# Kernel optimization log

Measured on AMD Instinct MI355X. Metric: run time of the kernel, lower is better.

## Reference

```python
import jax, jax.numpy as jnp
import numpy as np

B, N, D, H = 2, 256, 512, 8
DK = D // H


def _lin(x, w, b):
    # torch nn.Linear: y = x @ W.T + b, W is [out, in]
    return jnp.matmul(x, w.T) + b


def setup_inputs() -> dict:
    key = jax.random.key(0)
    ks = jax.random.split(key, 12)
    std = 0.02
    inp = {
        "x": jax.random.normal(ks[0], (B, N, D), jnp.float32),
        "batched_graphs": jax.random.normal(ks[1], (B, N, N, D), jnp.float32) * std,
        "mask": jnp.zeros((B, N, N), dtype=bool),
    }
    names = ["wq", "wk", "wv", "wo", "wl", "wr", "wrk", "wrv"]
    for i, n in enumerate(names):
        inp[n] = jax.random.normal(ks[2 + i], (D, D), jnp.float32) * std
        inp["b" + n[1:]] = jnp.zeros((D,), jnp.float32)
    return inp


def reference(x, batched_graphs, mask,
              wq, bq, wk, bk, wv, bv, wo, bo,
              wl, bl, wr, br, wrk, brk, wrv, brv):
    # update_relations: per-edge key/value maps
    graphs_k = _lin(batched_graphs, wrk, brk).reshape(B, N, N, H, DK)
    graphs_v = _lin(batched_graphs, wrv, brv).reshape(B, N, N, H, DK)

    query = _lin(x, wq, bq).reshape(B, N, H, DK)
    key_ = _lin(x, wk, bk).reshape(B, N, H, DK)
    value = _lin(x, wv, bv).reshape(B, N, H, DK)

    scores_k = jnp.einsum("bxhd,byhd->bxyh", query, key_)
    scores_g = jnp.einsum("bxhd,bxyhd->bxyh", query, graphs_k)
    scores = (scores_k + scores_g) / np.sqrt(DK).astype(np.float32)
    scores = jnp.where(mask[..., None], jnp.float32(-1e9), scores)
    p_attn = jax.nn.softmax(scores, axis=2)  # over key nodes y

    x_v = jnp.einsum("bxyh,byhd->bxhd", p_attn, value)
    x_g = jnp.einsum("bxyh,bxyhd->bxhd", p_attn, graphs_v)
    out = (x_v + x_g).reshape(B, N, D)

    # relation update: outer sum of left/right projections
    x_left = _lin(out, wl, bl)[:, :, None, :]   # [B,N,1,D]
    x_right = _lin(out, wr, br)[:, None, :, :]  # [B,1,N,D]
    new_graphs = x_left + x_right               # [B,N,N,D]

    return _lin(out, wo, bo), new_graphs
```

## Files before the change

### kernel.cpp

```cpp
#include <hip/hip_runtime.h>

#define BB 2
#define NN 256
#define DD 512
#define HH 8

typedef float f4raw __attribute__((ext_vector_type(4)));

__device__ __forceinline__ float dot4(float4 a, float4 b) {
    return a.x*b.x + a.y*b.y + a.z*b.z + a.w*b.w;
}

__device__ __forceinline__ float4 f4fma(float s, float4 a, float4 acc) {
    acc.x += s * a.x; acc.y += s * a.y; acc.z += s * a.z; acc.w += s * a.w;
    return acc;
}

__device__ __forceinline__ float4 f4mul(float s, float4 a) {
    a.x *= s; a.y *= s; a.z *= s; a.w *= s; return a;
}

__device__ __forceinline__ void gload_lds16(const void* g, void* l) {
    __builtin_amdgcn_global_load_lds(
        (const __attribute__((address_space(1))) unsigned int*)g,
        (__attribute__((address_space(3))) unsigned int*)l, 16, 0, 0);
}

__device__ __forceinline__ void stage_swz(const char* rowbase, float4* dst, int w, int lane) {
    #pragma unroll
    for (int j = 0; j < 4; ++j) {
        const int f0 = w * 256 + j * 64;
        const int y = f0 >> 7;
        const int c = (f0 & 127) + lane;
        gload_lds16(rowbase + (size_t)y * 2048 + ((size_t)(c ^ y) << 4), &dst[f0]);
    }
}

__device__ __forceinline__ void stageG(const char* Grow, int tt, int w, int lane, float4* dst) {
    #pragma unroll
    for (int r = 0; r < 2; ++r) {
        const int yr = 2 * w + r;
        const char* src = Grow + (size_t)(tt * 8 + yr) * 2048;
        #pragma unroll
        for (int j = 0; j < 2; ++j) {
            const int c = j * 64 + lane;
            gload_lds16(src + ((size_t)(c ^ yr) << 4), &dst[r * 128 + j * 64]);
        }
    }
}

__global__ __launch_bounds__(64) void kProj(
    const float* __restrict__ in_,
    const float* __restrict__ w0, const float* __restrict__ b0,
    const float* __restrict__ w1, const float* __restrict__ b1,
    const float* __restrict__ w2, const float* __restrict__ b2,
    float* __restrict__ o0, float* __restrict__ o1, float* __restrict__ o2)
{
    __shared__ float4 xs[2][32 * 5];
    __shared__ float4 ws[2][32 * 5];

    const int t = threadIdx.x;
    const int blk = blockIdx.x;
    const int proj = blk >> 8;
    const int rem = blk & 255;
    const int row0 = (rem >> 4) * 32;
    const int col0 = (rem & 15) * 32;

    const float* W; const float* Bp; float* O;
    if (proj == 0)      { W = w0; Bp = b0; O = o0; }
    else if (proj == 1) { W = w1; Bp = b1; O = o1; }
    else                { W = w2; Bp = b2; O = o2; }

    const float4* X4 = (const float4*)in_ + (size_t)row0 * 128;
    const float4* W4 = (const float4*)W  + (size_t)col0 * 128;

    const int sr = t >> 2, se = t & 3;
    const int ty = t >> 3, tx = t & 7;

    float4 rx0 = X4[(size_t)sr * 128 + se];
    float4 rx1 = X4[(size_t)(sr + 16) * 128 + se];
    float4 rw0 = W4[(size_t)sr * 128 + se];
    float4 rw1 = W4[(size_t)(sr + 16) * 128 + se];
    xs[0][sr * 5 + se] = rx0;  xs[0][(sr + 16) * 5 + se] = rx1;
    ws[0][sr * 5 + se] = rw0;  ws[0][(sr + 16) * 5 + se] = rw1;

    float acc[4][4] = {};

    for (int q = 0; q < 32; ++q) {
        __syncthreads();
        const int cur = q & 1;
        if (q < 31) {
            const int ko = (q + 1) * 4;
            rx0 = X4[(size_t)sr * 128 + ko + se];
            rx1 = X4[(size_t)(sr + 16) * 128 + ko + se];
            rw0 = W4[(size_t)sr * 128 + ko + se];
            rw1 = W4[(size_t)(sr + 16) * 128 + ko + se];
        }
        const float4* xb = xs[cur];
        const float4* wb = ws[cur];
        #pragma unroll
        for (int e4 = 0; e4 < 4; ++e4) {
            float4 xr[4], wc[4];
            #pragma unroll
            for (int i = 0; i < 4; ++i) xr[i] = xb[(ty + 8 * i) * 5 + e4];
            #pragma unroll
            for (int j = 0; j < 4; ++j) wc[j] = wb[(tx + 8 * j) * 5 + e4];
            #pragma unroll
            for (int i = 0; i < 4; ++i)
                #pragma unroll
                for (int j = 0; j < 4; ++j)
                    acc[i][j] += dot4(xr[i], wc[j]);
        }
        if (q < 31) {
            const int nxt = cur ^ 1;
            xs[nxt][sr * 5 + se] = rx0;  xs[nxt][(sr + 16) * 5 + se] = rx1;
            ws[nxt][sr * 5 + se] = rw0;  ws[nxt][(sr + 16) * 5 + se] = rw1;
        }
    }

    float bb[4];
    #pragma unroll
    for (int j = 0; j < 4; ++j) bb[j] = Bp[col0 + tx + 8 * j];
    #pragma unroll
    for (int i = 0; i < 4; ++i) {
        const int orow = row0 + ty + 8 * i;
        #pragma unroll
        for (int j = 0; j < 4; ++j)
            O[(size_t)orow * DD + col0 + tx + 8 * j] = acc[i][j] + bb[j];
    }
}

__global__ __launch_bounds__(256) void kQkp(
    const float* __restrict__ q, const float* __restrict__ wrk,
    float* __restrict__ qkp)
{
    __shared__ float qs[8 * 64];
    const int t = threadIdx.x;
    const int blk = blockIdx.x;
    const int rowg = blk >> 5;
    const int h = (blk >> 2) & 7;
    const int eq = blk & 3;
    const int row0 = rowg * 8;
    {
        const int r = t >> 5, d2 = (t & 31) * 2;
        const float2 tmp = *(const float2*)(q + (size_t)(row0 + r) * DD + h * 64 + d2);
        qs[r * 64 + d2] = tmp.x; qs[r * 64 + d2 + 1] = tmp.y;
    }
    __syncthreads();
    const int e = eq * 128 + (t & 127);
    const int rp = (t >> 7) * 4;
    const float* wcol = wrk + (size_t)(h * 64) * DD + e;
    float a0 = 0, a1 = 0, a2 = 0, a3 = 0;
    #pragma unroll 8
    for (int d = 0; d < 64; ++d) {
        const float wv = wcol[(size_t)d * DD];
        a0 += qs[(rp + 0) * 64 + d] * wv;
        a1 += qs[(rp + 1) * 64 + d] * wv;
        a2 += qs[(rp + 2) * 64 + d] * wv;
        a3 += qs[(rp + 3) * 64 + d] * wv;
    }
    qkp[((size_t)(row0 + rp + 0) * HH + h) * DD + e] = a0;
    qkp[((size_t)(row0 + rp + 1) * HH + h) * DD + e] = a1;
    qkp[((size_t)(row0 + rp + 2) * HH + h) * DD + e] = a2;
    qkp[((size_t)(row0 + rp + 3) * HH + h) * DD + e] = a3;
}

__global__ __launch_bounds__(256) void kSk(
    const float* __restrict__ q, const float* __restrict__ k,
    const unsigned char* __restrict__ mask, float* __restrict__ sk)
{
    __shared__ float qs[8 * 65];
    __shared__ float ks[64 * 65];
    const int t = threadIdx.x;
    const int blk = blockIdx.x;
    const int b  = blk >> 10;
    const int h  = (blk >> 7) & 7;
    const int xt = (blk >> 2) & 31;
    const int yt = blk & 3;
    const int x0 = xt * 8, y0 = yt * 64;
    {
        const int r = t >> 5, d2 = (t & 31) * 2;
        const float2 tmp = *(const float2*)(q + (size_t)(b * NN + x0 + r) * DD + h * 64 + d2);
        qs[r * 65 + d2] = tmp.x; qs[r * 65 + d2 + 1] = tmp.y;
    }
    #pragma unroll
    for (int j = 0; j < 8; ++j) {
        const int f = t + 256 * j;
        const int r = f >> 5, d2 = (f & 31) * 2;
        const float2 tmp = *(const float2*)(k + (size_t)(b * NN + y0 + r) * DD + h * 64 + d2);
        ks[r * 65 + d2] = tmp.x; ks[r * 65 + d2 + 1] = tmp.y;
    }
    __syncthreads();
    const int xi = t >> 5, yg = t & 31;
    float a0 = 0, a1 = 0;
    #pragma unroll 8
    for (int d = 0; d < 64; ++d) {
        const float qv = qs[xi * 65 + d];
        a0 += qv * ks[(yg * 2 + 0) * 65 + d];
        a1 += qv * ks[(yg * 2 + 1) * 65 + d];
    }
    a0 *= 0.125f; a1 *= 0.125f;
    const unsigned char* mrow = mask + (size_t)(b * NN + x0 + xi) * NN;
    const int gy = y0 + yg * 2;
    if (mrow[gy + 0]) a0 = -1e9f;
    if (mrow[gy + 1]) a1 = -1e9f;
    float2 st; st.x = a0; st.y = a1;
    *(float2*)(sk + ((size_t)(b * NN + x0 + xi) * HH + h) * NN + gy) = st;
}

__global__ __launch_bounds__(256, 2) void kC(
    const float* __restrict__ G, const float* __restrict__ sk,
    const float* __restrict__ qkp, const float* __restrict__ v,
    const float* __restrict__ wrv, const float* __restrict__ brv,
    float* __restrict__ om)
{
    __shared__ float4 Gdb[2][4][256];
    __shared__ float4 qk4[1024];
    __shared__ float  sk_l[2048];
    __shared__ float  s_st[2048];
    __shared__ float  ml[64];

    const int t = threadIdx.x;
    const int lane = t & 63;
    const int w = t >> 6;
    const int bid = blockIdx.x;
    const int b = bid >> 8;

    const char* Grow = (const char*)(G + (size_t)bid * NN * DD);

    stage_swz((const char*)(qkp + (size_t)bid * HH * DD), qk4, w, lane);
    {
        const char* skb = (const char*)(sk + (size_t)bid * HH * NN);
        gload_lds16(skb + (size_t)(w * 128 + lane) * 16,      (float4*)sk_l + w * 128);
        gload_lds16(skb + (size_t)(w * 128 + 64 + lane) * 16, (float4*)sk_l + w * 128 + 64);
    }
    stageG(Grow, 0, w, lane, &Gdb[0][w][0]);
    asm volatile("s_waitcnt vmcnt(4)" ::: "memory");
    __builtin_amdgcn_sched_barrier(0);
    __builtin_amdgcn_s_barrier();

    const int s_ = lane & 15;
    const int g  = lane >> 4;
    const int h0 = 2 * g;
    const int yr0 = 2 * w, yr1 = 2 * w + 1;

    float4 gA[8], gB[8];
    float m[8], l[8];
    #pragma unroll
    for (int h = 0; h < 8; ++h) {
        gA[h] = make_float4(0, 0, 0, 0); gB[h] = make_float4(0, 0, 0, 0);
        m[h] = -3e38f; l[h] = 0.f;
    }

    int cb = 0;
    #pragma unroll 1
    for (int tt = 0; tt < 32; ++tt) {
        __builtin_amdgcn_sched_barrier(0);
        if (tt < 31) {
            stageG(Grow, tt + 1, w, lane, &Gdb[cb ^ 1][w][0]);
            asm volatile("s_waitcnt vmcnt(4)" ::: "memory");
        } else {
            asm volatile("s_waitcnt vmcnt(0)" ::: "memory");
        }
        __builtin_amdgcn_sched_barrier(0);

        const float4* gb = &Gdb[cb][w][0];
        const int gy0 = tt * 8 + yr0, gy1 = tt * 8 + yr1;

        {
            float a00 = 0, a01 = 0, a10 = 0, a11 = 0;
            #pragma unroll
            for (int i = 0; i < 8; ++i) {
                const int e4 = i * 16 + s_;
                const float4 g0 = gb[(e4 ^ yr0)];
                const float4 g1 = gb[128 + (e4 ^ yr1)];
                const float4 p0 = qk4[h0 * 128 + (e4 ^ h0)];
                const float4 p1 = qk4[(h0 + 1) * 128 + (e4 ^ (h0 + 1))];
                a00 += dot4(g0, p0); a01 += dot4(g0, p1);
                a10 += dot4(g1, p0); a11 += dot4(g1, p1);
            }
            #pragma unroll
            for (int mm = 1; mm < 16; mm <<= 1) {
                a00 += __shfl_xor(a00, mm); a01 += __shfl_xor(a01, mm);
                a10 += __shfl_xor(a10, mm); a11 += __shfl_xor(a11, mm);
            }
            if (s_ < 4) {
                const int yy = s_ & 1, hh = s_ >> 1;
                const float val = yy ? (hh ? a11 : a10) : (hh ? a01 : a00);
                const int h = h0 + hh;
                const int gy = yy ? gy1 : gy0;
                s_st[gy * 8 + h] = val * 0.125f + sk_l[h * 256 + gy];
            }
        }

        const float4 sva = *(const float4*)&s_st[gy0 * 8];
        const float4 svb = *(const float4*)&s_st[gy0 * 8 + 4];
        const float4 svc = *(const float4*)&s_st[gy1 * 8];
        const float4 svd = *(const float4*)&s_st[gy1 * 8 + 4];
        const float s0[8] = {sva.x, sva.y, sva.z, sva.w, svb.x, svb.y, svb.z, svb.w};
        const float s1[8] = {svc.x, svc.y, svc.z, svc.w, svd.x, svd.y, svd.z, svd.w};

        const float4 gr0a = gb[(lane ^ yr0)];
        const float4 gr0b = gb[((lane + 64) ^ yr0)];
        const float4 gr1a = gb[128 + (lane ^ yr1)];
        const float4 gr1b = gb[128 + ((lane + 64) ^ yr1)];

        #pragma unroll
        for (int h = 0; h < 8; ++h) {
            const float mn = fmaxf(m[h], fmaxf(s0[h], s1[h]));
            const float rs = __expf(m[h] - mn);
            const float p0 = __expf(s0[h] - mn);
            const float p1 = __expf(s1[h] - mn);
            m[h] = mn;
            l[h] = l[h] * rs + p0 + p1;
            gA[h] = f4fma(p1, gr1a, f4fma(p0, gr0a, f4mul(rs, gA[h])));
            gB[h] = f4fma(p1, gr1b, f4fma(p0, gr0b, f4mul(rs, gB[h])));
        }
        cb ^= 1;
    }

    asm volatile("s_waitcnt vmcnt(0)" ::: "memory");
    __syncthreads();
    if (lane == 0) {
        #pragma unroll
        for (int h = 0; h < 8; ++h) { ml[w * 16 + h] = m[h]; ml[w * 16 + 8 + h] = l[h]; }
    }
    __syncthreads();

    float M[8], Lf[8];
    #pragma unroll
    for (int h = 0; h < 8; ++h) {
        const float m0 = ml[h], m1 = ml[16 + h], m2 = ml[32 + h], m3 = ml[48 + h];
        const float mm = fmaxf(fmaxf(m0, m1), fmaxf(m2, m3));
        M[h] = mm;
        Lf[h] = __expf(m0 - mm) * ml[8 + h]  + __expf(m1 - mm) * ml[24 + h]
              + __expf(m2 - mm) * ml[40 + h] + __expf(m3 - mm) * ml[56 + h];
    }
    #pragma unroll
    for (int h = 0; h < 8; ++h) {
        const float ws = __expf(m[h] - M[h]);
        gA[h] = f4mul(ws, gA[h]); gB[h] = f4mul(ws, gB[h]);
    }
    float4* rA = &Gdb[0][0][0];
    float4* rB = &Gdb[1][0][0];
    if (w == 2) {
        #pragma unroll
        for (int h = 0; h < 8; ++h) { rA[h * 128 + lane] = gA[h]; rA[h * 128 + 64 + lane] = gB[h]; }
    }
    if (w == 3) {
        #pragma unroll
        for (int h = 0; h < 8; ++h) { rB[h * 128 + lane] = gA[h]; rB[h * 128 + 64 + lane] = gB[h]; }
    }
    __syncthreads();
    if (w == 0) {
        #pragma unroll
        for (int h = 0; h < 8; ++h) {
            gA[h].x += rA[h*128+lane].x; gA[h].y += rA[h*128+lane].y; gA[h].z += rA[h*128+lane].z; gA[h].w += rA[h*128+lane].w;
            gB[h].x += rA[h*128+64+lane].x; gB[h].y += rA[h*128+64+lane].y; gB[h].z += rA[h*128+64+lane].z; gB[h].w += rA[h*128+64+lane].w;
        }
    }
    if (w == 1) {
        #pragma unroll
        for (int h = 0; h < 8; ++h) {
            gA[h].x += rB[h*128+lane].x; gA[h].y += rB[h*128+lane].y; gA[h].z += rB[h*128+lane].z; gA[h].w += rB[h*128+lane].w;
            gB[h].x += rB[h*128+64+lane].x; gB[h].y += rB[h*128+64+lane].y; gB[h].z += rB[h*128+64+lane].z; gB[h].w += rB[h*128+64+lane].w;
        }
    }
    __syncthreads();
    if (w == 1) {
        #pragma unroll
        for (int h = 0; h < 8; ++h) { rA[h * 128 + lane] = gA[h]; rA[h * 128 + 64 + lane] = gB[h]; }
    }
    __syncthreads();
    if (w == 0) {
        #pragma unroll
        for (int h = 0; h < 8; ++h) {
            gA[h].x += rA[h*128+lane].x; gA[h].y += rA[h*128+lane].y; gA[h].z += rA[h*128+lane].z; gA[h].w += rA[h*128+lane].w;
            gB[h].x += rA[h*128+64+lane].x; gB[h].y += rA[h*128+64+lane].y; gB[h].z += rA[h*128+64+lane].z; gB[h].w += rA[h*128+64+lane].w;
            qk4[h * 128 + lane] = gA[h];
            qk4[h * 128 + 64 + lane] = gB[h];
        }
    }
    if (t == 0) {
        #pragma unroll
        for (int h = 0; h < 8; ++h) ml[h] = Lf[h];
    }
    {
        #pragma unroll
        for (int h = 0; h < 8; ++h) sk_l[t * 8 + h] = __expf(s_st[t * 8 + h] - M[h]);
    }
    __syncthreads();

    const float* vb = v + (size_t)(b * NN) * DD;
    #pragma unroll
    for (int jj = 0; jj < 2; ++jj) {
        const int o = jj * 256 + t;
        const int h = o >> 6, d = o & 63;
        const float4* wr4 = (const float4*)(wrv + (size_t)o * DD);
        const float4* gf = (const float4*)qk4 + h * 128;
        float acc = 0;
        #pragma unroll 4
        for (int e4 = 0; e4 < 128; ++e4) acc += dot4(wr4[e4], gf[e4]);
        float xv = 0;
        const float* vc = vb + h * 64 + d;
        #pragma unroll 4
        for (int y = 0; y < 256; ++y) xv += sk_l[y * 8 + h] * vc[(size_t)y * DD];
        om[(size_t)bid * DD + o] = (xv + acc) / ml[h] + brv[o];
    }
}

__global__ __launch_bounds__(256) void kE(
    const float* __restrict__ xl, const float* __restrict__ xr,
    float* __restrict__ ng)
{
    const int t = threadIdx.x;
    const int blk = blockIdx.x;
    const int bid = blk >> 2;
    const int yc = blk & 3;
    const int b = bid >> 8;
    const int o4 = t & 127;
    const int yh = t >> 7;
    const float4 left = ((const float4*)xl)[(size_t)bid * 128 + o4];
    const float4* xr4 = (const float4*)xr + (size_t)b * NN * 128;
    f4raw* out4 = (f4raw*)ng + (size_t)bid * NN * 128;
    for (int y = yc * 64 + yh; y < yc * 64 + 64; y += 2) {
        const float4 rr = xr4[y * 128 + o4];
        f4raw s;
        s.x = left.x + rr.x; s.y = left.y + rr.y;
        s.z = left.z + rr.z; s.w = left.w + rr.w;
        __builtin_nontemporal_store(s, &out4[y * 128 + o4]);
    }
}

extern "C" void kernel_launch(void* const* d_in, const int* in_sizes, int n_in,
                              void* d_out, int out_size, void* d_ws, size_t ws_size,
                              hipStream_t stream)
{
    (void)in_sizes; (void)n_in; (void)out_size; (void)ws_size;
    const float* x    = (const float*)d_in[0];
    const float* G    = (const float*)d_in[1];
    const unsigned char* mask = (const unsigned char*)d_in[2];
    const float* wq  = (const float*)d_in[3];  const float* bq  = (const float*)d_in[4];
    const float* wk  = (const float*)d_in[5];  const float* bk  = (const float*)d_in[6];
    const float* wv  = (const float*)d_in[7];  const float* bv  = (const float*)d_in[8];
    const float* wo  = (const float*)d_in[9];  const float* bo  = (const float*)d_in[10];
    const float* wl  = (const float*)d_in[11]; const float* bl  = (const float*)d_in[12];
    const float* wr  = (const float*)d_in[13]; const float* br  = (const float*)d_in[14];
    const float* wrk = (const float*)d_in[15];
    const float* wrv = (const float*)d_in[17]; const float* brv = (const float*)d_in[18];

    float* out  = (float*)d_out;
    float* fout = out;
    float* ng   = out + (size_t)BB * NN * DD;

    const size_t ng_f  = (size_t)BB * NN * NN * DD;
    const size_t row_f = (size_t)BB * NN * DD;
    const size_t total = row_f * 16;
    float* base = ng + ng_f - total;
    float* q    = base;
    float* k    = q   + row_f;
    float* vv_  = k   + row_f;
    float* qkp  = vv_ + row_f;
    float* skp  = qkp + row_f * 8;
    float* om   = skp + row_f * 4;
    float* xl = (float*)d_ws;
    float* xr = xl + row_f;

    kProj<<<768, 64, 0, stream>>>(x, wq, bq, wk, bk, wv, bv, q, k, vv_);
    kQkp <<<2048, 256, 0, stream>>>(q, wrk, qkp);
    kSk  <<<2048, 256, 0, stream>>>(q, k, mask, skp);
    kC   <<<512, 256, 0, stream>>>(G, skp, qkp, vv_, wrv, brv, om);
    kProj<<<768, 64, 0, stream>>>(om, wo, bo, wl, bl, wr, br, fout, xl, xr);
    kE   <<<2048, 256, 0, stream>>>(xl, xr, ng);
}
```

Before: 291.4 us.

## Split attention over key chunks with flash-decoding style merge kernel

The main attention kernel kC now splits each query row's 256 keys into four 64-key partitions, launching 2048 blocks instead of 512. Each block writes partial graph-weighted sums, value sums, running max and denominators. A new kernel kM merges the four partials with rescaled exponentials and applies the wrv projection and bias. The value accumulation also moves into the streaming loop, replacing the separate post-loop pass over v. This raises parallelism on the bandwidth-bound G stream, at the cost of an extra launch and about 32 row-sized partial buffers written to and read from global scratch.

```diff
diff --git a/kernel.cpp b/kernel.cpp
--- a/kernel.cpp
+++ b/kernel.cpp
@@ -18,6 +18,10 @@
 
 __device__ __forceinline__ float4 f4mul(float s, float4 a) {
     a.x *= s; a.y *= s; a.z *= s; a.w *= s; return a;
+}
+
+__device__ __forceinline__ float4 f4add(float4 a, float4 b) {
+    a.x += b.x; a.y += b.y; a.z += b.z; a.w += b.w; return a;
 }
 
 __device__ __forceinline__ void gload_lds16(const void* g, void* l) {
@@ -211,61 +215,71 @@
 __global__ __launch_bounds__(256, 2) void kC(
     const float* __restrict__ G, const float* __restrict__ sk,
     const float* __restrict__ qkp, const float* __restrict__ v,
-    const float* __restrict__ wrv, const float* __restrict__ brv,
-    float* __restrict__ om)
+    float* __restrict__ pg, float* __restrict__ pxv,
+    float* __restrict__ pm, float* __restrict__ pl)
 {
     __shared__ float4 Gdb[2][4][256];
     __shared__ float4 qk4[1024];
-    __shared__ float  sk_l[2048];
-    __shared__ float  s_st[2048];
-    __shared__ float  ml[64];
+    __shared__ float  sk_lds[512];
+    __shared__ float  s_st[512];
 
     const int t = threadIdx.x;
     const int lane = t & 63;
     const int w = t >> 6;
-    const int bid = blockIdx.x;
+    const int blk = blockIdx.x;
+    const int part = blk & 3;
+    const int bid = blk >> 2;
     const int b = bid >> 8;
-
-    const char* Grow = (const char*)(G + (size_t)bid * NN * DD);
-
+    const int ybase = part * 64;
+
+    const int s_ = lane & 15;
+    const int g  = lane >> 4;
+    const int h0_ = 2 * g, h1_ = h0_ + 1;
+    const int yr0 = 2 * w, yr1 = yr0 + 1;
+
+    const char* Grow = (const char*)(G + (size_t)bid * NN * DD) + (size_t)ybase * 2048;
+    const float* skb = sk + (size_t)bid * HH * NN;
+    const float4* vb4 = (const float4*)(v + (size_t)(b * NN) * DD);
+
+    const int f0p = 2 * t, f1p = 2 * t + 1;
+    const float skv0 = skb[(f0p & 7) * NN + ybase + (f0p >> 3)];
+    const float skv1 = skb[(f1p & 7) * NN + ybase + (f1p >> 3)];
     stage_swz((const char*)(qkp + (size_t)bid * HH * DD), qk4, w, lane);
-    {
-        const char* skb = (const char*)(sk + (size_t)bid * HH * NN);
-        gload_lds16(skb + (size_t)(w * 128 + lane) * 16,      (float4*)sk_l + w * 128);
-        gload_lds16(skb + (size_t)(w * 128 + 64 + lane) * 16, (float4*)sk_l + w * 128 + 64);
-    }
     stageG(Grow, 0, w, lane, &Gdb[0][w][0]);
     asm volatile("s_waitcnt vmcnt(4)" ::: "memory");
     __builtin_amdgcn_sched_barrier(0);
-    __builtin_amdgcn_s_barrier();
-
-    const int s_ = lane & 15;
-    const int g  = lane >> 4;
-    const int h0 = 2 * g;
-    const int yr0 = 2 * w, yr1 = 2 * w + 1;
+    sk_lds[f0p] = skv0;
+    sk_lds[f1p] = skv1;
+    __syncthreads();
 
     float4 gA[8], gB[8];
     float m[8], l[8];
     #pragma unroll
     for (int h = 0; h < 8; ++h) {
-        gA[h] = make_float4(0, 0, 0, 0); gB[h] = make_float4(0, 0, 0, 0);
+        gA[h] = make_float4(0, 0, 0, 0);
+        gB[h] = make_float4(0, 0, 0, 0);
         m[h] = -3e38f; l[h] = 0.f;
     }
+    float4 xva = {0, 0, 0, 0}, xvb = {0, 0, 0, 0};
 
     int cb = 0;
     #pragma unroll 1
-    for (int tt = 0; tt < 32; ++tt) {
+    for (int tt = 0; tt < 8; ++tt) {
+        const int gy0 = ybase + tt * 8 + yr0;
+        const int gy1 = gy0 + 1;
+        const int ry0 = tt * 8 + yr0, ry1 = ry0 + 1;
+
+        const float4 va0 = vb4[(size_t)gy0 * 128 + 32 * g + s_];
+        const float4 vb0 = vb4[(size_t)gy0 * 128 + 32 * g + 16 + s_];
+        const float4 va1 = vb4[(size_t)gy1 * 128 + 32 * g + s_];
+        const float4 vb1 = vb4[(size_t)gy1 * 128 + 32 * g + 16 + s_];
         __builtin_amdgcn_sched_barrier(0);
-        if (tt < 31) {
+        if (tt < 7)
             stageG(Grow, tt + 1, w, lane, &Gdb[cb ^ 1][w][0]);
-            asm volatile("s_waitcnt vmcnt(4)" ::: "memory");
-        } else {
-            asm volatile("s_waitcnt vmcnt(0)" ::: "memory");
-        }
+        asm volatile("s_waitcnt vmcnt(4)" ::: "memory");
         __builtin_amdgcn_sched_barrier(0);
 
         const float4* gb = &Gdb[cb][w][0];
-        const int gy0 = tt * 8 + yr0, gy1 = tt * 8 + yr1;
 
         {
             float a00 = 0, a01 = 0, a10 = 0, a11 = 0;
@@ -274,8 +288,8 @@
                 const int e4 = i * 16 + s_;
                 const float4 g0 = gb[(e4 ^ yr0)];
                 const float4 g1 = gb[128 + (e4 ^ yr1)];
-                const float4 p0 = qk4[h0 * 128 + (e4 ^ h0)];
-                const float4 p1 = qk4[(h0 + 1) * 128 + (e4 ^ (h0 + 1))];
+                const float4 p0 = qk4[h0_ * 128 + (e4 ^ h0_)];
+                const float4 p1 = qk4[h1_ * 128 + (e4 ^ h1_)];
                 a00 += dot4(g0, p0); a01 += dot4(g0, p1);
                 a10 += dot4(g1, p0); a11 += dot4(g1, p1);
             }
@@ -287,16 +301,16 @@
             if (s_ < 4) {
                 const int yy = s_ & 1, hh = s_ >> 1;
                 const float val = yy ? (hh ? a11 : a10) : (hh ? a01 : a00);
-                const int h = h0 + hh;
-                const int gy = yy ? gy1 : gy0;
-                s_st[gy * 8 + h] = val * 0.125f + sk_l[h * 256 + gy];
+                const int h = h0_ + hh;
+                const int ry = yy ? ry1 : ry0;
+                s_st[ry * 8 + h] = val * 0.125f + sk_lds[ry * 8 + h];
             }
         }
 
-        const float4 sva = *(const float4*)&s_st[gy0 * 8];
-        const float4 svb = *(const float4*)&s_st[gy0 * 8 + 4];
-        const float4 svc = *(const float4*)&s_st[gy1 * 8];
-        const float4 svd = *(const float4*)&s_st[gy1 * 8 + 4];
+        const float4 sva = *(const float4*)&s_st[ry0 * 8];
+        const float4 svb = *(const float4*)&s_st[ry0 * 8 + 4];
+        const float4 svc = *(const float4*)&s_st[ry1 * 8];
+        const float4 svd = *(const float4*)&s_st[ry1 * 8 + 4];
         const float s0[8] = {sva.x, sva.y, sva.z, sva.w, svb.x, svb.y, svb.z, svb.w};
         const float s1[8] = {svc.x, svc.y, svc.z, svc.w, svd.x, svd.y, svd.z, svd.w};
 
@@ -305,6 +319,7 @@
         const float4 gr1a = gb[128 + (lane ^ yr1)];
         const float4 gr1b = gb[128 + ((lane + 64) ^ yr1)];
 
+        float p0a = 0, p1a = 0, rsa = 1, p0b = 0, p1b = 0, rsb = 1;
         #pragma unroll
         for (int h = 0; h < 8; ++h) {
             const float mn = fmaxf(m[h], fmaxf(s0[h], s1[h]));
@@ -315,34 +330,46 @@
             l[h] = l[h] * rs + p0 + p1;
             gA[h] = f4fma(p1, gr1a, f4fma(p0, gr0a, f4mul(rs, gA[h])));
             gB[h] = f4fma(p1, gr1b, f4fma(p0, gr0b, f4mul(rs, gB[h])));
-        }
+            if (h == h0_) { p0a = p0; p1a = p1; rsa = rs; }
+            if (h == h1_) { p0b = p0; p1b = p1; rsb = rs; }
+        }
+        xva = f4fma(p1a, va1, f4fma(p0a, va0, f4mul(rsa, xva)));
+        xvb = f4fma(p1b, vb1, f4fma(p0b, vb0, f4mul(rsb, xvb)));
         cb ^= 1;
     }
 
     asm volatile("s_waitcnt vmcnt(0)" ::: "memory");
     __syncthreads();
+    float* ml = sk_lds;
     if (lane == 0) {
         #pragma unroll
         for (int h = 0; h < 8; ++h) { ml[w * 16 + h] = m[h]; ml[w * 16 + 8 + h] = l[h]; }
     }
     __syncthreads();
 
-    float M[8], Lf[8];
+    float ea = 1.f, eb = 1.f;
+    float Mv[8], Lv[8];
     #pragma unroll
     for (int h = 0; h < 8; ++h) {
-        const float m0 = ml[h], m1 = ml[16 + h], m2 = ml[32 + h], m3 = ml[48 + h];
-        const float mm = fmaxf(fmaxf(m0, m1), fmaxf(m2, m3));
-        M[h] = mm;
-        Lf[h] = __expf(m0 - mm) * ml[8 + h]  + __expf(m1 - mm) * ml[24 + h]
-              + __expf(m2 - mm) * ml[40 + h] + __expf(m3 - mm) * ml[56 + h];
-    }
-    #pragma unroll
-    for (int h = 0; h < 8; ++h) {
-        const float ws = __expf(m[h] - M[h]);
-        gA[h] = f4mul(ws, gA[h]); gB[h] = f4mul(ws, gB[h]);
-    }
+        const float q0 = ml[h], q1 = ml[16 + h], q2 = ml[32 + h], q3 = ml[48 + h];
+        const float Mh = fmaxf(fmaxf(q0, q1), fmaxf(q2, q3));
+        const float Lh = __expf(q0 - Mh) * ml[8 + h]  + __expf(q1 - Mh) * ml[24 + h]
+                       + __expf(q2 - Mh) * ml[40 + h] + __expf(q3 - Mh) * ml[56 + h];
+        Mv[h] = Mh; Lv[h] = Lh;
+        const float e = __expf(m[h] - Mh);
+        gA[h] = f4mul(e, gA[h]);
+        gB[h] = f4mul(e, gB[h]);
+        if (h == h0_) ea = e;
+        if (h == h1_) eb = e;
+    }
+    xva = f4mul(ea, xva);
+    xvb = f4mul(eb, xvb);
+
     float4* rA = &Gdb[0][0][0];
     float4* rB = &Gdb[1][0][0];
+    float4* xs_ = qk4;
+    xs_[w * 128 + 32 * g + s_] = xva;
+    xs_[w * 128 + 32 * g + 16 + s_] = xvb;
     if (w == 2) {
         #pragma unroll
         for (int h = 0; h < 8; ++h) { rA[h * 128 + lane] = gA[h]; rA[h * 128 + 64 + lane] = gB[h]; }
@@ -355,15 +382,15 @@
     if (w == 0) {
         #pragma unroll
         for (int h = 0; h < 8; ++h) {
-            gA[h].x += rA[h*128+lane].x; gA[h].y += rA[h*128+lane].y; gA[h].z += rA[h*128+lane].z; gA[h].w += rA[h*128+lane].w;
-            gB[h].x += rA[h*128+64+lane].x; gB[h].y += rA[h*128+64+lane].y; gB[h].z += rA[h*128+64+lane].z; gB[h].w += rA[h*128+64+lane].w;
+            gA[h] = f4add(gA[h], rA[h * 128 + lane]);
+            gB[h] = f4add(gB[h], rA[h * 128 + 64 + lane]);
         }
     }
     if (w == 1) {
         #pragma unroll
         for (int h = 0; h < 8; ++h) {
-            gA[h].x += rB[h*128+lane].x; gA[h].y += rB[h*128+lane].y; gA[h].z += rB[h*128+lane].z; gA[h].w += rB[h*128+lane].w;
-            gB[h].x += rB[h*128+64+lane].x; gB[h].y += rB[h*128+64+lane].y; gB[h].z += rB[h*128+64+lane].z; gB[h].w += rB[h*128+64+lane].w;
+            gA[h] = f4add(gA[h], rB[h * 128 + lane]);
+            gB[h] = f4add(gB[h], rB[h * 128 + 64 + lane]);
         }
     }
     __syncthreads();
@@ -373,40 +400,92 @@
     }
     __syncthreads();
     if (w == 0) {
+        float4* pgb = (float4*)pg + (size_t)blk * 1024;
         #pragma unroll
         for (int h = 0; h < 8; ++h) {
-            gA[h].x += rA[h*128+lane].x; gA[h].y += rA[h*128+lane].y; gA[h].z += rA[h*128+lane].z; gA[h].w += rA[h*128+lane].w;
-            gB[h].x += rA[h*128+64+lane].x; gB[h].y += rA[h*128+64+lane].y; gB[h].z += rA[h*128+64+lane].z; gB[h].w += rA[h*128+64+lane].w;
-            qk4[h * 128 + lane] = gA[h];
-            qk4[h * 128 + 64 + lane] = gB[h];
-        }
-    }
-    if (t == 0) {
-        #pragma unroll
-        for (int h = 0; h < 8; ++h) ml[h] = Lf[h];
+            gA[h] = f4add(gA[h], rA[h * 128 + lane]);
+            gB[h] = f4add(gB[h], rA[h * 128 + 64 + lane]);
+            pgb[h * 128 + lane] = gA[h];
+            pgb[h * 128 + 64 + lane] = gB[h];
+        }
+        float4 xa = f4add(f4add(xs_[32 * g + s_],            xs_[128 + 32 * g + s_]),
+                          f4add(xs_[256 + 32 * g + s_],      xs_[384 + 32 * g + s_]));
+        float4 xb = f4add(f4add(xs_[32 * g + 16 + s_],       xs_[128 + 32 * g + 16 + s_]),
+                          f4add(xs_[256 + 32 * g + 16 + s_], xs_[384 + 32 * g + 16 + s_]));
+        float4* pxb = (float4*)pxv + (size_t)blk * 128;
+        pxb[32 * g + s_] = xa;
+        pxb[32 * g + 16 + s_] = xb;
+        if (lane == 0) {
+            #pragma unroll
+            for (int h = 0; h < 8; ++h) { pm[blk * 8 + h] = Mv[h]; pl[blk * 8 + h] = Lv[h]; }
+        }
+    }
+}
+
+__global__ __launch_bounds__(256) void kM(
+    const float* __restrict__ pg, const float* __restrict__ pxv,
+    const float* __restrict__ pm, const float* __restrict__ pl,
+    const float* __restrict__ wrv, const float* __restrict__ brv,
+    float* __restrict__ om)
+{
+    __shared__ float4 gc[512];
+    __shared__ float xvs[256];
+    __shared__ float wexp[16], Ls[4];
+    const int t = threadIdx.x;
+    const int blk = blockIdx.x;
+    const int bid = blk >> 1;
+    const int half = blk & 1;
+    const int h0 = half * 4;
+    __shared__ float mlds[16], llds[16];
+    if (t < 16) {
+        const int i = t >> 2, hh = t & 3;
+        mlds[t] = pm[bid * 32 + i * 8 + h0 + hh];
+        llds[t] = pl[bid * 32 + i * 8 + h0 + hh];
+    }
+    __syncthreads();
+    if (t < 4) {
+        float M = mlds[t];
+        #pragma unroll
+        for (int i = 1; i < 4; ++i) M = fmaxf(M, mlds[i * 4 + t]);
+        float L = 0;
+        #pragma unroll
+        for (int i = 0; i < 4; ++i) {
+            const float wv = __expf(mlds[i * 4 + t] - M);
+            wexp[i * 4 + t] = wv;
+            L += wv * llds[i * 4 + t];
+        }
+        Ls[t] = L;
+    }
+    __syncthreads();
+    const int c4 = t & 127;
+    #pragma unroll
+    for (int r = 0; r < 2; ++r) {
+        const int hh = (t >> 7) * 2 + r;
+        float4 acc = {0, 0, 0, 0};
+        #pragma unroll
+        for (int i = 0; i < 4; ++i) {
+            const float wv = wexp[i * 4 + hh];
+            const float4 g = ((const float4*)pg)[((size_t)bid * 4 + i) * 1024 + (size_t)(h0 + hh) * 128 + c4];
+            acc.x += wv * g.x; acc.y += wv * g.y; acc.z += wv * g.z; acc.w += wv * g.w;
+        }
+        gc[hh * 128 + c4] = acc;
     }
     {
-        #pragma unroll
-        for (int h = 0; h < 8; ++h) sk_l[t * 8 + h] = __expf(s_st[t * 8 + h] - M[h]);
-    }
-    __syncthreads();
-
-    const float* vb = v + (size_t)(b * NN) * DD;
-    #pragma unroll
-    for (int jj = 0; jj < 2; ++jj) {
-        const int o = jj * 256 + t;
-        const int h = o >> 6, d = o & 63;
-        const float4* wr4 = (const float4*)(wrv + (size_t)o * DD);
-        const float4* gf = (const float4*)qk4 + h * 128;
-        float acc = 0;
-        #pragma unroll 4
-        for (int e4 = 0; e4 < 128; ++e4) acc += dot4(wr4[e4], gf[e4]);
-        float xv = 0;
-        const float* vc = vb + h * 64 + d;
-        #pragma unroll 4
-        for (int y = 0; y < 256; ++y) xv += sk_l[y * 8 + h] * vc[(size_t)y * DD];
-        om[(size_t)bid * DD + o] = (xv + acc) / ml[h] + brv[o];
-    }
+        const int hh = t >> 6;
+        float s = 0;
+        #pragma unroll
+        for (int i = 0; i < 4; ++i)
+            s += wexp[i * 4 + hh] * pxv[((size_t)bid * 4 + i) * DD + half * 256 + t];
+        xvs[t] = s;
+    }
+    __syncthreads();
+    const int o = half * 256 + t;
+    const int hl = t >> 6;
+    const float4* wr4 = (const float4*)(wrv + (size_t)o * DD);
+    float acc = 0;
+    #pragma unroll 4
+    for (int e4 = 0; e4 < 128; ++e4) acc += dot4(wr4[e4], gc[hl * 128 + e4]);
+    om[(size_t)bid * DD + o] = (xvs[t] + acc) / Ls[hl] + brv[o];
 }
 
 __global__ __launch_bounds__(256) void kE(
@@ -455,21 +534,26 @@
 
     const size_t ng_f  = (size_t)BB * NN * NN * DD;
     const size_t row_f = (size_t)BB * NN * DD;
-    const size_t total = row_f * 16;
+    const size_t total = row_f * 52 + 32768;
     float* base = ng + ng_f - total;
     float* q    = base;
     float* k    = q   + row_f;
     float* vv_  = k   + row_f;
     float* qkp  = vv_ + row_f;
     float* skp  = qkp + row_f * 8;
-    float* om   = skp + row_f * 4;
+    float* pg   = skp + row_f * 4;
+    float* pxv  = pg  + row_f * 32;
+    float* pm   = pxv + row_f * 4;
+    float* pl   = pm  + 16384;
+    float* om   = pl  + 16384;
     float* xl = (float*)d_ws;
     float* xr = xl + row_f;
 
     kProj<<<768, 64, 0, stream>>>(x, wq, bq, wk, bk, wv, bv, q, k, vv_);
     kQkp <<<2048, 256, 0, stream>>>(q, wrk, qkp);
     kSk  <<<2048, 256, 0, stream>>>(q, k, mask, skp);
-    kC   <<<512, 256, 0, stream>>>(G, skp, qkp, vv_, wrv, brv, om);
+    kC   <<<2048, 256, 0, stream>>>(G, skp, qkp, vv_, pg, pxv, pm, pl);
+    kM   <<<1024, 256, 0, stream>>>(pg, pxv, pm, pl, wrv, brv, om);
     kProj<<<768, 64, 0, stream>>>(om, wo, bo, wl, bl, wr, br, fout, xl, xr);
     kE   <<<2048, 256, 0, stream>>>(xl, xr, ng);
 }
```

Measured after the change: 295.7 us. Within noise of the previous version (+1.5%).
